# Optimization experiments

Hardware: AMD Instinct MI355X
Metric: run time of the kernel (lower is better)

## Reference

```python
import jax, jax.numpy as jnp
import numpy as np

B, N, M = 4, 2048, 2048
D_IN1, D_IN2 = 512, 512
H, DK, DV = 8, 64, 64


def setup_inputs() -> dict:
    key = jax.random.key(0)
    ks = jax.random.split(key, 8)
    s = 0.02
    return {
        "first_seq": jax.random.normal(ks[0], (B, N, D_IN1), jnp.float32),
        "second_seq": jax.random.normal(ks[1], (B, M, D_IN2), jnp.float32),
        # Linear params stored as (in, out); y = x @ W + b
        "Wq": jax.random.normal(ks[2], (D_IN1, H * DK), jnp.float32) * s,
        "bq": jnp.zeros((H * DK,), jnp.float32),
        "Wk": jax.random.normal(ks[3], (D_IN2, H * DK), jnp.float32) * s,
        "bk": jnp.zeros((H * DK,), jnp.float32),
        "Wv": jax.random.normal(ks[4], (D_IN2, H * DV), jnp.float32) * s,
        "bv": jnp.zeros((H * DV,), jnp.float32),
    }


def reference(first_seq, second_seq, Wq, bq, Wk, bk, Wv, bv):
    # projections, then split heads: (B, L, H*D) -> (B, L, H, D)
    q = (first_seq @ Wq + bq).reshape(B, N, H, DK)
    k = (second_seq @ Wk + bk).reshape(B, M, H, DK)
    v = (second_seq @ Wv + bv).reshape(B, M, H, DV)
    scores = jnp.einsum("bnhd,bmhd->bhnm", q, k) / np.sqrt(DK).astype(np.float32)
    attn = jax.nn.softmax(scores, axis=-1)
    # output keeps separated heads, matching the original module: (B, N, H, DV)
    out = jnp.einsum("bhnm,bmhd->bnhd", attn, v)
    return out
```

## Files before the change

kernel.cpp:

```cpp
#include <hip/hip_runtime.h>
#include <hip/hip_bf16.h>


#define B_  4
#define N_  2048
#define M_  2048
#define HD  512

#define QSCALE 0.18033688011112042f

typedef __attribute__((ext_vector_type(8)))  short bf16x8;
typedef __attribute__((ext_vector_type(16))) float f32x16;
typedef __attribute__((ext_vector_type(4)))  float f32x4;
typedef __attribute__((ext_vector_type(4)))  unsigned int u32x4;
typedef __attribute__((ext_vector_type(2)))  unsigned int u32x2;

__device__ __forceinline__ unsigned short f2bf(float f) {
  unsigned int u = __float_as_uint(f);
  u += 0x7fffu + ((u >> 16) & 1u);
  return (unsigned short)(u >> 16);
}

__device__ __forceinline__ void gl16(const unsigned short* g, unsigned short* l) {
  __builtin_amdgcn_global_load_lds(
      (const __attribute__((address_space(1))) void*)g,
      (__attribute__((address_space(3))) void*)l, 16, 0, 0);
}

__device__ __forceinline__ unsigned int cvtpk(float lo, float hi) {
  unsigned int r;
  asm("v_cvt_pk_bf16_f32 %0, %1, %2" : "=v"(r) : "v"(lo), "v"(hi));
  return r;
}

__global__ __launch_bounds__(256) void wt_kernel(
    const float* __restrict__ Wq, const float* __restrict__ Wk,
    const float* __restrict__ Wv, unsigned short* __restrict__ WtAll)
{
  __shared__ float Lf[64 * 65];
  const int z  = blockIdx.z;
  const float* W = (z == 0) ? Wq : (z == 1) ? Wk : Wv;
  unsigned short* Wt = WtAll + (size_t)z * 512 * 512;
  const int k0 = blockIdx.x * 64, n0 = blockIdx.y * 64;
  const int tid = threadIdx.x;
  {
    const int row4 = (tid >> 4) * 4;
    const int c4   = (tid & 15) * 4;
#pragma unroll
    for (int r = 0; r < 4; ++r) {
      float4 v = *(const float4*)(W + (size_t)(k0 + row4 + r) * 512 + n0 + c4);
      Lf[(row4 + r) * 65 + c4 + 0] = v.x;
      Lf[(row4 + r) * 65 + c4 + 1] = v.y;
      Lf[(row4 + r) * 65 + c4 + 2] = v.z;
      Lf[(row4 + r) * 65 + c4 + 3] = v.w;
    }
  }
  __syncthreads();
  {
    const int nl = tid >> 2;
    const int ks = (tid & 3) * 16;
    unsigned int pk[8];
#pragma unroll
    for (int j = 0; j < 8; ++j)
      pk[j] = cvtpk(Lf[(ks + 2 * j) * 65 + nl], Lf[(ks + 2 * j + 1) * 65 + nl]);
    u32x4 lo = {pk[0], pk[1], pk[2], pk[3]};
    u32x4 hi = {pk[4], pk[5], pk[6], pk[7]};
    *(u32x4*)(Wt + (size_t)(n0 + nl) * 512 + k0 + ks)     = lo;
    *(u32x4*)(Wt + (size_t)(n0 + nl) * 512 + k0 + ks + 8) = hi;
  }
}

__global__ __launch_bounds__(256, 3) void gemm_kernel(
    const float* __restrict__ first, const float* __restrict__ second,
    const unsigned short* __restrict__ WtAll,
    const float* __restrict__ bq, const float* __restrict__ bk,
    const float* __restrict__ bv,
    unsigned short* __restrict__ qws, unsigned short* __restrict__ kws,
    unsigned short* __restrict__ vtw)
{
  __shared__ __align__(16) unsigned short smem[24576];

  const int tid  = threadIdx.x;
  const int lane = tid & 63;
  const int w    = tid >> 6;
  const int wr   = w >> 1, wc = w & 1;
  const int c16  = lane & 15;
  const int hi   = lane >> 4;
  const int kb8  = 8 * hi;

  const int z = blockIdx.z;
  const float* X = (z == 0) ? first : second;
  const unsigned short* Wt = WtAll + (size_t)z * 262144;
  const float* bias = (z == 0) ? bq : (z == 1) ? bk : bv;
  const float oscale = (z == 0) ? QSCALE : 1.0f;

  const int r0 = blockIdx.x * 128;
  const int n0 = blockIdx.y * 128;

  const f32x4 z4 = {0.f, 0.f, 0.f, 0.f};
  f32x4 acc[4][4] = {{z4,z4,z4,z4},{z4,z4,z4,z4},{z4,z4,z4,z4},{z4,z4,z4,z4}};

  const int ar = tid >> 2;
  const int ac = (tid & 3) * 16;
  float4 xa[2][4];

  auto loadA = [&](int kb) {
#pragma unroll
    for (int h2 = 0; h2 < 2; ++h2)
#pragma unroll
      for (int j = 0; j < 4; ++j)
        xa[h2][j] = *(const float4*)(X + (size_t)(r0 + h2 * 64 + ar) * 512 + kb + ac + 4 * j);
  };
  auto writeA = [&]() {
    unsigned short* As = smem;
#pragma unroll
    for (int h2 = 0; h2 < 2; ++h2) {
      const int row = h2 * 64 + ar;
      u32x4 lo = { cvtpk(xa[h2][0].x, xa[h2][0].y), cvtpk(xa[h2][0].z, xa[h2][0].w),
                   cvtpk(xa[h2][1].x, xa[h2][1].y), cvtpk(xa[h2][1].z, xa[h2][1].w) };
      u32x4 hi4= { cvtpk(xa[h2][2].x, xa[h2][2].y), cvtpk(xa[h2][2].z, xa[h2][2].w),
                   cvtpk(xa[h2][3].x, xa[h2][3].y), cvtpk(xa[h2][3].z, xa[h2][3].w) };
      const int g0 = (ac >> 3) ^ (row & 7);
      *(u32x4*)&As[row * 64 + (g0 << 3)]        = lo;
      *(u32x4*)&As[row * 64 + ((g0 ^ 1) << 3)]  = hi4;
    }
  };
  auto stageB = [&](int bufi, int kb) {
    unsigned short* Bs = smem + 8192 + bufi * 8192;
#pragma unroll
    for (int s = 0; s < 4; ++s) {
      const int n = s * 32 + (tid >> 3);
      gl16(Wt + (size_t)(n0 + n) * 512 + kb + ((8 * (tid & 7)) ^ ((n & 7) << 3)),
           Bs + s * 2048 + tid * 8);
    }
  };

  loadA(0);
  writeA();
  stageB(0, 0);
  __syncthreads();

  int buf = 0;
#pragma unroll 1
  for (int t = 0; t < 8; ++t) {
    if (t < 7) { stageB(buf ^ 1, (t + 1) * 64); loadA((t + 1) * 64); }
    const unsigned short* As = smem;
    const unsigned short* Bs = smem + 8192 + buf * 8192;
#pragma unroll
    for (int kk = 0; kk < 64; kk += 32) {
      bf16x8 a[4], bfr[4];
#pragma unroll
      for (int i = 0; i < 4; ++i) {
        const int row = 64 * wr + 16 * i + c16;
        a[i] = *(const bf16x8*)&As[row * 64 + ((kk + kb8) ^ ((row & 7) << 3))];
      }
#pragma unroll
      for (int j = 0; j < 4; ++j) {
        const int n = 64 * wc + 16 * j + c16;
        bfr[j] = *(const bf16x8*)&Bs[n * 64 + ((kk + kb8) ^ ((n & 7) << 3))];
      }
#pragma unroll
      for (int i = 0; i < 4; ++i)
#pragma unroll
        for (int j = 0; j < 4; ++j)
          acc[i][j] = __builtin_amdgcn_mfma_f32_16x16x32_bf16(a[i], bfr[j], acc[i][j], 0, 0, 0);
    }
    __builtin_amdgcn_s_barrier();
    if (t < 7) writeA();
    __syncthreads();
    buf ^= 1;
  }

  const int hcol0 = n0 + 64 * wc;
  if (z < 2) {
    unsigned short* Y = (z == 0) ? qws : kws;
#pragma unroll
    for (int j = 0; j < 4; ++j) {
      const int colg = hcol0 + 16 * j + c16;
      const float bv_ = bias[colg];
#pragma unroll
      for (int i = 0; i < 4; ++i) {
        const int rowb = r0 + 64 * wr + 16 * i + 4 * hi;
#pragma unroll
        for (int r = 0; r < 4; ++r)
          Y[(size_t)(rowb + r) * 512 + colg] = f2bf((acc[i][j][r] + bv_) * oscale);
      }
    }
  } else {
    unsigned short* T = smem + w * 4608;
#pragma unroll
    for (int j = 0; j < 4; ++j) {
      const int n = 16 * j + c16;
      const float bv_ = bias[hcol0 + n];
#pragma unroll
      for (int i = 0; i < 4; ++i) {
        const int m = 16 * i + 4 * hi;
        u32x2 p = { cvtpk(acc[i][j][0] + bv_, acc[i][j][1] + bv_),
                    cvtpk(acc[i][j][2] + bv_, acc[i][j][3] + bv_) };
        const int gg = (m >> 3) ^ (n & 7);
        *(u32x2*)&T[n * 72 + gg * 8 + (m & 7)] = p;
      }
    }
    __builtin_amdgcn_s_waitcnt(0);
    const int b_  = r0 >> 11;
    const int m0g = (r0 + 64 * wr) & 2047;
    const int h_  = hcol0 >> 6;
    const int mc  = lane & 7;
#pragma unroll
    for (int p = 0; p < 8; ++p) {
      const int nr = 8 * p + (lane >> 3);
      bf16x8 v = *(const bf16x8*)&T[nr * 72 + ((mc ^ (nr & 7)) << 3)];
      *(bf16x8*)(vtw + ((size_t)((b_ * 8 + h_) * 64 + nr) * 2048 + m0g + mc * 8)) = v;
    }
  }
}

__global__ __launch_bounds__(512, 4) void attn_kernel(
    const unsigned short* __restrict__ Qw, const unsigned short* __restrict__ Kw,
    const unsigned short* __restrict__ Vtg, float* __restrict__ Out)
{
  __shared__ __align__(16) unsigned short smem[32768];

  const int tid  = threadIdx.x;
  const int lane = tid & 63;
  const int w    = tid >> 6;
  const int wq   = w & 3;
  const int ms   = w >> 2;
  const int q32  = lane & 31;
  const int g    = lane >> 5;
  const int g8   = g * 8;
  const int rsw  = (q32 & 7) << 3;

  const int bh = blockIdx.y;
  const int b  = bh >> 3;
  const int h  = bh & 7;

  const unsigned short* Kb  = Kw  + (size_t)b * M_ * HD + h * 64;
  const unsigned short* Vtb = Vtg + (size_t)bh * 64 * 2048;

  const int q0 = blockIdx.x * 128 + wq * 32;
  const unsigned short* Qb = Qw + ((size_t)b * N_ + q0 + q32) * HD + h * 64;

  bf16x8 qf[4];
#pragma unroll
  for (int c = 0; c < 4; ++c)
    qf[c] = *(const bf16x8*)(Qb + 16 * c + g8);

  f32x16 oA = {0,0,0,0,0,0,0,0,0,0,0,0,0,0,0,0};
  f32x16 oB = {0,0,0,0,0,0,0,0,0,0,0,0,0,0,0,0};
  float lr = 0.f;

  const int srow = tid >> 3;
  const int sce  = (8 * (tid & 7)) ^ ((srow & 7) << 3);

  auto stage = [&](int bufi, int m0A, int m0B) {
    gl16(Kb  + (size_t)(m0A + srow) * HD + sce,  &smem[(0 | bufi) * 4096 + tid * 8]);
    gl16(Vtb + (size_t)srow * 2048 + m0A + sce,  &smem[(2 | bufi) * 4096 + tid * 8]);
    gl16(Kb  + (size_t)(m0B + srow) * HD + sce,  &smem[(4 | bufi) * 4096 + tid * 8]);
    gl16(Vtb + (size_t)srow * 2048 + m0B + sce,  &smem[(6 | bufi) * 4096 + tid * 8]);
  };

  stage(0, 0, 1024);
  __syncthreads();

  int buf = 0;
  const int NT = M_ / 128;
  for (int t = 0; t < NT; ++t) {
    if (t + 1 < NT) stage(buf ^ 1, (t + 1) * 64, 1024 + (t + 1) * 64);
    const unsigned short* Kt = &smem[((ms << 2) | buf) * 4096];
    const unsigned short* Vt = &smem[((ms << 2) | 2 | buf) * 4096];

    f32x16 s0 = {0,0,0,0,0,0,0,0,0,0,0,0,0,0,0,0};
    f32x16 s1 = {0,0,0,0,0,0,0,0,0,0,0,0,0,0,0,0};
    __builtin_amdgcn_s_setprio(1);
#pragma unroll
    for (int c = 0; c < 4; ++c) {
      const int col = (16 * c + g8) ^ rsw;
      bf16x8 a0 = *(const bf16x8*)&Kt[q32 * 64 + col];
      bf16x8 a1 = *(const bf16x8*)&Kt[(32 + q32) * 64 + col];
      s0 = __builtin_amdgcn_mfma_f32_32x32x16_bf16(a0, qf[c], s0, 0, 0, 0);
      s1 = __builtin_amdgcn_mfma_f32_32x32x16_bf16(a1, qf[c], s1, 0, 0, 0);
    }
    __builtin_amdgcn_s_setprio(0);

    unsigned int A0[4], B0[4], A1[4], B1[4];
    float ts = 0.f;
#pragma unroll
    for (int k = 0; k < 4; ++k) {
      float e0 = __builtin_amdgcn_exp2f(s0[4*k+0]), e1 = __builtin_amdgcn_exp2f(s0[4*k+1]);
      float e2 = __builtin_amdgcn_exp2f(s0[4*k+2]), e3 = __builtin_amdgcn_exp2f(s0[4*k+3]);
      ts += (e0 + e1) + (e2 + e3);
      A0[k] = cvtpk(e0, e1);  B0[k] = cvtpk(e2, e3);
      float f0 = __builtin_amdgcn_exp2f(s1[4*k+0]), f1 = __builtin_amdgcn_exp2f(s1[4*k+1]);
      float f2 = __builtin_amdgcn_exp2f(s1[4*k+2]), f3 = __builtin_amdgcn_exp2f(s1[4*k+3]);
      ts += (f0 + f1) + (f2 + f3);
      A1[k] = cvtpk(f0, f1);  B1[k] = cvtpk(f2, f3);
    }
    lr += ts;

    bf16x8 pb[4];
#pragma unroll
    for (int tt = 0; tt < 2; ++tt) {
      asm volatile("v_permlane32_swap_b32 %0, %1" : "+v"(A0[2*tt]), "+v"(A0[2*tt+1]));
      asm volatile("v_permlane32_swap_b32 %0, %1" : "+v"(B0[2*tt]), "+v"(B0[2*tt+1]));
      u32x4 pc = { A0[2*tt], B0[2*tt], A0[2*tt+1], B0[2*tt+1] };
      pb[tt] = __builtin_bit_cast(bf16x8, pc);
      asm volatile("v_permlane32_swap_b32 %0, %1" : "+v"(A1[2*tt]), "+v"(A1[2*tt+1]));
      asm volatile("v_permlane32_swap_b32 %0, %1" : "+v"(B1[2*tt]), "+v"(B1[2*tt+1]));
      u32x4 qc = { A1[2*tt], B1[2*tt], A1[2*tt+1], B1[2*tt+1] };
      pb[2 + tt] = __builtin_bit_cast(bf16x8, qc);
    }

    __builtin_amdgcn_s_setprio(1);
#pragma unroll
    for (int c = 0; c < 4; ++c) {
      const int col = (16 * c + g8) ^ rsw;
      bf16x8 v0 = *(const bf16x8*)&Vt[q32 * 64 + col];
      bf16x8 v1 = *(const bf16x8*)&Vt[(32 + q32) * 64 + col];
      oA = __builtin_amdgcn_mfma_f32_32x32x16_bf16(v0, pb[c], oA, 0, 0, 0);
      oB = __builtin_amdgcn_mfma_f32_32x32x16_bf16(v1, pb[c], oB, 0, 0, 0);
    }
    __builtin_amdgcn_s_setprio(0);

    __syncthreads();
    buf ^= 1;
  }

  float* Pf = (float*)smem;
  if (w >= 4) {
    float* Pw_ = Pf + (size_t)(w - 4) * 2112 + lane * 33;
#pragma unroll
    for (int i = 0; i < 16; ++i) { Pw_[i] = oA[i]; Pw_[16 + i] = oB[i]; }
    Pw_[32] = lr;
  }
  __syncthreads();

  float* Of = (float*)smem;
  if (w < 4) {
    float* Pw_ = Pf + (size_t)w * 2112 + lane * 33;
#pragma unroll
    for (int i = 0; i < 16; ++i) { oA[i] += Pw_[i]; oB[i] += Pw_[16 + i]; }
    lr += Pw_[32];
    lr += __shfl_xor(lr, 32);
    const float linv = 1.f / lr;
#pragma unroll
    for (int i = 0; i < 16; ++i) { oA[i] *= linv; oB[i] *= linv; }
  }
  __syncthreads();

  if (w < 4) {
    const int ql_w = w * 32 + q32;
#pragma unroll
    for (int k = 0; k < 4; ++k) {
#pragma unroll
      for (int r = 0; r < 4; ++r) {
        const int dv = r + 8 * k + 4 * g;
        Of[dv * 129 + ql_w]        = oA[4*k+r];
        Of[(32 + dv) * 129 + ql_w] = oB[4*k+r];
      }
    }
  }
  __syncthreads();

  const int ql = tid >> 2;
  const int dh = (tid & 3) * 16;
  float* Og = Out + ((size_t)b * N_ + blockIdx.x * 128 + ql) * HD + h * 64 + dh;
#pragma unroll
  for (int j = 0; j < 16; j += 4) {
    float4 v = { Of[(dh + j) * 129 + ql],     Of[(dh + j + 1) * 129 + ql],
                 Of[(dh + j + 2) * 129 + ql], Of[(dh + j + 3) * 129 + ql] };
    *(float4*)(Og + j) = v;
  }
}

extern "C" void kernel_launch(void* const* d_in, const int* in_sizes, int n_in,
                              void* d_out, int out_size, void* d_ws, size_t ws_size,
                              hipStream_t stream) {
  (void)in_sizes; (void)n_in; (void)out_size; (void)ws_size;
  const float* first  = (const float*)d_in[0];
  const float* second = (const float*)d_in[1];
  const float* Wq = (const float*)d_in[2];
  const float* bq = (const float*)d_in[3];
  const float* Wk = (const float*)d_in[4];
  const float* bk = (const float*)d_in[5];
  const float* Wv = (const float*)d_in[6];
  const float* bv = (const float*)d_in[7];

  unsigned short* qws = (unsigned short*)d_ws;
  unsigned short* kws = qws + (size_t)8192 * 512;
  unsigned short* vtw = kws + (size_t)8192 * 512;
  unsigned short* wts = vtw + (size_t)8192 * 512;

  wt_kernel<<<dim3(8, 8, 3), dim3(256), 0, stream>>>(Wq, Wk, Wv, wts);
  gemm_kernel<<<dim3(64, 4, 3), dim3(256), 0, stream>>>(
      first, second, wts, bq, bk, bv, qws, kws, vtw);
  attn_kernel<<<dim3(16, 32), dim3(512), 0, stream>>>(qws, kws, vtw, (float*)d_out);
}
```

Baseline: 78.48 us.

## Use 512-thread GEMM blocks and compute softmax row sums via ones-MFMA

The projection GEMM moves from 4 to 8 waves per 128x128 tile. Each wave now owns a 64x32 sub-tile, and loading of A and staging of B are split over twice as many threads, with the transposed-V epilogue offset to match. In the attention kernel, the per-lane scalar sum of exponentials is replaced by an extra 32x32x16 MFMA against a vector of bf16 ones, which removes the VALU adds and the cross-half shuffle. The sum now uses bf16-rounded probabilities, and the attention occupancy hint is lowered from 4 to 2 blocks per SM.

Result: no change. 79.12 us (+0.8%).

```diff
diff --git a/kernel.cpp b/kernel.cpp
--- a/kernel.cpp
+++ b/kernel.cpp
@@ -70,7 +70,7 @@
   }
 }
 
-__global__ __launch_bounds__(256, 3) void gemm_kernel(
+__global__ __launch_bounds__(512, 2) void gemm_kernel(
     const float* __restrict__ first, const float* __restrict__ second,
     const unsigned short* __restrict__ WtAll,
     const float* __restrict__ bq, const float* __restrict__ bk,
@@ -83,7 +83,7 @@
   const int tid  = threadIdx.x;
   const int lane = tid & 63;
   const int w    = tid >> 6;
-  const int wr   = w >> 1, wc = w & 1;
+  const int wr   = w >> 2, wc = w & 3;
   const int c16  = lane & 15;
   const int hi   = lane >> 4;
   const int kb8  = 8 * hi;
@@ -98,40 +98,34 @@
   const int n0 = blockIdx.y * 128;
 
   const f32x4 z4 = {0.f, 0.f, 0.f, 0.f};
-  f32x4 acc[4][4] = {{z4,z4,z4,z4},{z4,z4,z4,z4},{z4,z4,z4,z4},{z4,z4,z4,z4}};
+  f32x4 acc[4][2] = {{z4,z4},{z4,z4},{z4,z4},{z4,z4}};
 
   const int ar = tid >> 2;
   const int ac = (tid & 3) * 16;
-  float4 xa[2][4];
+  float4 xa[4];
 
   auto loadA = [&](int kb) {
 #pragma unroll
-    for (int h2 = 0; h2 < 2; ++h2)
-#pragma unroll
-      for (int j = 0; j < 4; ++j)
-        xa[h2][j] = *(const float4*)(X + (size_t)(r0 + h2 * 64 + ar) * 512 + kb + ac + 4 * j);
+    for (int j = 0; j < 4; ++j)
+      xa[j] = *(const float4*)(X + (size_t)(r0 + ar) * 512 + kb + ac + 4 * j);
   };
   auto writeA = [&]() {
     unsigned short* As = smem;
-#pragma unroll
-    for (int h2 = 0; h2 < 2; ++h2) {
-      const int row = h2 * 64 + ar;
-      u32x4 lo = { cvtpk(xa[h2][0].x, xa[h2][0].y), cvtpk(xa[h2][0].z, xa[h2][0].w),
-                   cvtpk(xa[h2][1].x, xa[h2][1].y), cvtpk(xa[h2][1].z, xa[h2][1].w) };
-      u32x4 hi4= { cvtpk(xa[h2][2].x, xa[h2][2].y), cvtpk(xa[h2][2].z, xa[h2][2].w),
-                   cvtpk(xa[h2][3].x, xa[h2][3].y), cvtpk(xa[h2][3].z, xa[h2][3].w) };
-      const int g0 = (ac >> 3) ^ (row & 7);
-      *(u32x4*)&As[row * 64 + (g0 << 3)]        = lo;
-      *(u32x4*)&As[row * 64 + ((g0 ^ 1) << 3)]  = hi4;
-    }
+    u32x4 lo = { cvtpk(xa[0].x, xa[0].y), cvtpk(xa[0].z, xa[0].w),
+                 cvtpk(xa[1].x, xa[1].y), cvtpk(xa[1].z, xa[1].w) };
+    u32x4 hi4= { cvtpk(xa[2].x, xa[2].y), cvtpk(xa[2].z, xa[2].w),
+                 cvtpk(xa[3].x, xa[3].y), cvtpk(xa[3].z, xa[3].w) };
+    const int g0 = (ac >> 3) ^ (ar & 7);
+    *(u32x4*)&As[ar * 64 + (g0 << 3)]        = lo;
+    *(u32x4*)&As[ar * 64 + ((g0 ^ 1) << 3)]  = hi4;
   };
   auto stageB = [&](int bufi, int kb) {
     unsigned short* Bs = smem + 8192 + bufi * 8192;
 #pragma unroll
-    for (int s = 0; s < 4; ++s) {
-      const int n = s * 32 + (tid >> 3);
+    for (int s = 0; s < 2; ++s) {
+      const int n = s * 64 + (tid >> 3);
       gl16(Wt + (size_t)(n0 + n) * 512 + kb + ((8 * (tid & 7)) ^ ((n & 7) << 3)),
-           Bs + s * 2048 + tid * 8);
+           Bs + s * 4096 + tid * 8);
     }
   };
 
@@ -148,21 +142,21 @@
     const unsigned short* Bs = smem + 8192 + buf * 8192;
 #pragma unroll
     for (int kk = 0; kk < 64; kk += 32) {
-      bf16x8 a[4], bfr[4];
+      bf16x8 a[4], bfr[2];
 #pragma unroll
       for (int i = 0; i < 4; ++i) {
         const int row = 64 * wr + 16 * i + c16;
         a[i] = *(const bf16x8*)&As[row * 64 + ((kk + kb8) ^ ((row & 7) << 3))];
       }
 #pragma unroll
-      for (int j = 0; j < 4; ++j) {
-        const int n = 64 * wc + 16 * j + c16;
+      for (int j = 0; j < 2; ++j) {
+        const int n = 32 * wc + 16 * j + c16;
         bfr[j] = *(const bf16x8*)&Bs[n * 64 + ((kk + kb8) ^ ((n & 7) << 3))];
       }
 #pragma unroll
       for (int i = 0; i < 4; ++i)
 #pragma unroll
-        for (int j = 0; j < 4; ++j)
+        for (int j = 0; j < 2; ++j)
           acc[i][j] = __builtin_amdgcn_mfma_f32_16x16x32_bf16(a[i], bfr[j], acc[i][j], 0, 0, 0);
     }
     __builtin_amdgcn_s_barrier();
@@ -171,11 +165,11 @@
     buf ^= 1;
   }
 
-  const int hcol0 = n0 + 64 * wc;
+  const int hcol0 = n0 + 32 * wc;
   if (z < 2) {
     unsigned short* Y = (z == 0) ? qws : kws;
 #pragma unroll
-    for (int j = 0; j < 4; ++j) {
+    for (int j = 0; j < 2; ++j) {
       const int colg = hcol0 + 16 * j + c16;
       const float bv_ = bias[colg];
 #pragma unroll
@@ -187,9 +181,9 @@
       }
     }
   } else {
-    unsigned short* T = smem + w * 4608;
-#pragma unroll
-    for (int j = 0; j < 4; ++j) {
+    unsigned short* T = smem + w * 2304;
+#pragma unroll
+    for (int j = 0; j < 2; ++j) {
       const int n = 16 * j + c16;
       const float bv_ = bias[hcol0 + n];
 #pragma unroll
@@ -205,17 +199,18 @@
     const int b_  = r0 >> 11;
     const int m0g = (r0 + 64 * wr) & 2047;
     const int h_  = hcol0 >> 6;
+    const int dvb = hcol0 & 63;
     const int mc  = lane & 7;
 #pragma unroll
-    for (int p = 0; p < 8; ++p) {
+    for (int p = 0; p < 4; ++p) {
       const int nr = 8 * p + (lane >> 3);
       bf16x8 v = *(const bf16x8*)&T[nr * 72 + ((mc ^ (nr & 7)) << 3)];
-      *(bf16x8*)(vtw + ((size_t)((b_ * 8 + h_) * 64 + nr) * 2048 + m0g + mc * 8)) = v;
-    }
-  }
-}
-
-__global__ __launch_bounds__(512, 4) void attn_kernel(
+      *(bf16x8*)(vtw + ((size_t)((b_ * 8 + h_) * 64 + dvb + nr) * 2048 + m0g + mc * 8)) = v;
+    }
+  }
+}
+
+__global__ __launch_bounds__(512, 2) void attn_kernel(
     const unsigned short* __restrict__ Qw, const unsigned short* __restrict__ Kw,
     const unsigned short* __restrict__ Vtg, float* __restrict__ Out)
 {
@@ -246,9 +241,13 @@
   for (int c = 0; c < 4; ++c)
     qf[c] = *(const bf16x8*)(Qb + 16 * c + g8);
 
+  const short one_bf = (short)0x3F80;
+  const bf16x8 vones = {one_bf, one_bf, one_bf, one_bf,
+                        one_bf, one_bf, one_bf, one_bf};
+
   f32x16 oA = {0,0,0,0,0,0,0,0,0,0,0,0,0,0,0,0};
   f32x16 oB = {0,0,0,0,0,0,0,0,0,0,0,0,0,0,0,0};
-  float lr = 0.f;
+  f32x16 lacc = {0,0,0,0,0,0,0,0,0,0,0,0,0,0,0,0};
 
   const int srow = tid >> 3;
   const int sce  = (8 * (tid & 7)) ^ ((srow & 7) << 3);
@@ -284,19 +283,15 @@
     __builtin_amdgcn_s_setprio(0);
 
     unsigned int A0[4], B0[4], A1[4], B1[4];
-    float ts = 0.f;
 #pragma unroll
     for (int k = 0; k < 4; ++k) {
       float e0 = __builtin_amdgcn_exp2f(s0[4*k+0]), e1 = __builtin_amdgcn_exp2f(s0[4*k+1]);
       float e2 = __builtin_amdgcn_exp2f(s0[4*k+2]), e3 = __builtin_amdgcn_exp2f(s0[4*k+3]);
-      ts += (e0 + e1) + (e2 + e3);
       A0[k] = cvtpk(e0, e1);  B0[k] = cvtpk(e2, e3);
       float f0 = __builtin_amdgcn_exp2f(s1[4*k+0]), f1 = __builtin_amdgcn_exp2f(s1[4*k+1]);
       float f2 = __builtin_amdgcn_exp2f(s1[4*k+2]), f3 = __builtin_amdgcn_exp2f(s1[4*k+3]);
-      ts += (f0 + f1) + (f2 + f3);
       A1[k] = cvtpk(f0, f1);  B1[k] = cvtpk(f2, f3);
     }
-    lr += ts;
 
     bf16x8 pb[4];
 #pragma unroll
@@ -319,12 +314,15 @@
       bf16x8 v1 = *(const bf16x8*)&Vt[(32 + q32) * 64 + col];
       oA = __builtin_amdgcn_mfma_f32_32x32x16_bf16(v0, pb[c], oA, 0, 0, 0);
       oB = __builtin_amdgcn_mfma_f32_32x32x16_bf16(v1, pb[c], oB, 0, 0, 0);
+      lacc = __builtin_amdgcn_mfma_f32_32x32x16_bf16(vones, pb[c], lacc, 0, 0, 0);
     }
     __builtin_amdgcn_s_setprio(0);
 
     __syncthreads();
     buf ^= 1;
   }
+
+  const float lr = lacc[0];
 
   float* Pf = (float*)smem;
   if (w >= 4) {
@@ -338,13 +336,13 @@
   float* Of = (float*)smem;
   if (w < 4) {
     float* Pw_ = Pf + (size_t)w * 2112 + lane * 33;
-#pragma unroll
-    for (int i = 0; i < 16; ++i) { oA[i] += Pw_[i]; oB[i] += Pw_[16 + i]; }
-    lr += Pw_[32];
-    lr += __shfl_xor(lr, 32);
-    const float linv = 1.f / lr;
-#pragma unroll
-    for (int i = 0; i < 16; ++i) { oA[i] *= linv; oB[i] *= linv; }
+    float lt = lr + Pw_[32];
+    const float linv = 1.f / lt;
+#pragma unroll
+    for (int i = 0; i < 16; ++i) {
+      oA[i] = (oA[i] + Pw_[i]) * linv;
+      oB[i] = (oB[i] + Pw_[16 + i]) * linv;
+    }
   }
   __syncthreads();
 
@@ -392,7 +390,7 @@
   unsigned short* wts = vtw + (size_t)8192 * 512;
 
   wt_kernel<<<dim3(8, 8, 3), dim3(256), 0, stream>>>(Wq, Wk, Wv, wts);
-  gemm_kernel<<<dim3(64, 4, 3), dim3(256), 0, stream>>>(
+  gemm_kernel<<<dim3(64, 4, 3), dim3(512), 0, stream>>>(
       first, second, wts, bq, bk, bv, qws, kws, vtw);
   attn_kernel<<<dim3(16, 32), dim3(512), 0, stream>>>(qws, kws, vtw, (float*)d_out);
 }
```
